# Kernel optimization log

Hardware: AMD Instinct MI355X
Metric: run time of the kernel (lower is better)

The kernel has to match this reference:

```python
import jax, jax.numpy as jnp
import numpy as np

MARGIN = 0.0
GAP = 0.4
N, D, C = 8192, 128, 10


def setup_inputs() -> dict:
    key = jax.random.key(0)
    k1, k2, k3 = jax.random.split(key, 3)
    inputs = jax.random.normal(k1, (N, D), dtype=jnp.float32)
    pred = jax.random.normal(k2, (N, C), dtype=jnp.float32)
    targets = jax.random.randint(k3, (N,), 0, C, dtype=jnp.int64)
    return {"inputs": inputs, "pred": pred, "targets": targets}


def reference(inputs, pred, targets):
    n = inputs.shape[0]
    # pairwise euclidean distances: ||xi||^2 + ||xj||^2 - 2 xi.xj, clamped + sqrt
    sq = jnp.sum(inputs * inputs, axis=1)                      # [n]
    dist = sq[:, None] + sq[None, :] - 2.0 * (inputs @ inputs.T)
    dist = jnp.sqrt(jnp.clip(dist, 1e-12))                     # [n, n]
    same = targets[:, None] == targets[None, :]                # [n, n] bool

    # confusion detection (original runs under no_grad)
    p = jax.nn.softmax(jax.lax.stop_gradient(pred), axis=1)
    val, top2 = jax.lax.top_k(p, 2)                            # [n,2]
    confuse = (val[:, 0] - val[:, 1] <= GAP) | (top2[:, 0] != targets)  # [n]

    # hard mining per row: hardest positive (max over same-class), hardest negative (min over diff-class)
    dist_ap = jnp.max(jnp.where(same, dist, -jnp.inf), axis=1)  # [n]
    dist_an = jnp.min(jnp.where(same, jnp.inf, dist), axis=1)   # [n]

    # MarginRankingLoss(margin=MARGIN) with y=1: mean(relu(-(an - ap) + margin)) over confused rows
    per_row = jnp.maximum(dist_ap - dist_an + MARGIN, 0.0)
    cnt = jnp.sum(confuse.astype(jnp.float32))
    loss = jnp.sum(jnp.where(confuse, per_row, 0.0)) / jnp.maximum(cnt, 1.0)
    return jnp.where(cnt > 0, loss, 0.0)
```

## Files before the change

kernel.cpp:

```cpp
#include <hip/hip_runtime.h>

#define NROWS 8192
#define DIMX  128
#define KB    192
#define KSEG  12
#define PTB   24576
#define NKS   3
#define NCLS  10
#define GAPV  0.4f
#define DEBIAS 504.03125f
#define SCL   (-0.0078125f)
#define RGR   256
#define NRG   (NROWS / RGR)
#define CHUNK 512
#define NCHUNK (NROWS / CHUNK)
#define SLAB  64
#define NSLAB (CHUNK / SLAB)

typedef __attribute__((ext_vector_type(4))) int i32x4;

#define GLOAD_LDS16(g, l)                                              \
  __builtin_amdgcn_global_load_lds(                                    \
      (const __attribute__((address_space(1))) void*)(g),              \
      (__attribute__((address_space(3))) void*)(l), 16, 0, 0)

__device__ __forceinline__ int q8(float v) {
  int q = (int)rintf(16.f * v);
  return q > 127 ? 127 : (q < -127 ? -127 : q);
}

__global__ __launch_bounds__(256) void prep_k(const float* __restrict__ x,
                                              const int* __restrict__ tgt,
                                              const float* __restrict__ pred,
                                              char* __restrict__ xa,
                                              char* __restrict__ xbm,
                                              float* __restrict__ sq,
                                              int* __restrict__ conf,
                                              unsigned* __restrict__ ctrs) {
  if (blockIdx.x == 0 && threadIdx.x < 3) ctrs[threadIdx.x] = 0u;

  const int wave = threadIdx.x >> 6;
  const int lane = threadIdx.x & 63;
  const int row  = blockIdx.x * 4 + wave;
  const float2 f2 = ((const float2*)(x + (size_t)row * DIMX))[lane];
  float s = f2.x * f2.x + f2.y * f2.y;
  #pragma unroll
  for (int m = 1; m < 64; m <<= 1) s += __shfl_xor(s, m, 64);

  char* basea = xa  + (size_t)(row >> 7) * PTB + (size_t)(row & 127) * 16;
  char* baseb = xbm + (size_t)(row >> 7) * PTB + (size_t)(row & 127) * 16;
  {
    const int q0 = q8(f2.x), q1 = q8(f2.y);
    const unsigned short u = (unsigned short)((q0 & 0xFF) | ((q1 & 0xFF) << 8));
    const size_t off = (size_t)(lane >> 3) * 2048 + (lane & 7) * 2;
    *(unsigned short*)(basea + off) = u;
    *(unsigned short*)(baseb + off) = u;
  }
  const int cls = tgt[row];
  if (lane < 32) {
    const int j = 2 * lane;
    const int c = j >> 2;
    const bool hit = (c < NCLS) && (c == cls);
    const unsigned short ua = hit ? (unsigned short)0x7F7F : 0;
    const unsigned short ub = hit ? (unsigned short)0x8181 : 0;
    const size_t off = (size_t)(8 + (j >> 4)) * 2048 + (j & 15);
    *(unsigned short*)(basea + off) = ua;
    *(unsigned short*)(baseb + off) = ub;
  }

  if (lane == 0) {
    sq[row] = s;
    const float* pp = pred + (size_t)row * NCLS;
    float v[NCLS];
    #pragma unroll
    for (int c = 0; c < NCLS; ++c) v[c] = pp[c];
    float m1 = v[0]; int i1 = 0;
    #pragma unroll
    for (int c = 1; c < NCLS; ++c)
      if (v[c] > m1) { m1 = v[c]; i1 = c; }
    float m2 = -INFINITY, sum = 0.f;
    #pragma unroll
    for (int c = 0; c < NCLS; ++c) {
      sum += __expf(v[c] - m1);
      if (c != i1) m2 = fmaxf(m2, v[c]);
    }
    const float d01 = (1.f - __expf(m2 - m1)) / sum;
    conf[row] = (d01 <= GAPV) || (i1 != cls);
  }
}

__global__ __launch_bounds__(256, 2) void gram_k(const char* __restrict__ xa,
                                                 const char* __restrict__ xbm,
                                                 const float* __restrict__ sq,
                                                 float* __restrict__ smax,
                                                 float* __restrict__ smin) {
  __shared__ char  ldsb[2][KSEG * 1024];
  __shared__ float sqb[2][SLAB];
  const int tid  = threadIdx.x;
  const int wave = tid >> 6;
  const int lane = tid & 63;
  const int quad = lane >> 4;
  const int m16  = lane & 15;
  const int bx = blockIdx.x, by = blockIdx.y;

  i32x4 A[4][NKS];
  #pragma unroll
  for (int rt = 0; rt < 4; ++rt) {
    const int rbase = wave * 64 + rt * 16;
    const char* pa = xa + (size_t)(bx * 2 + (rbase >> 7)) * PTB
                        + (size_t)((rbase & 127) + m16) * 16;
    #pragma unroll
    for (int ks = 0; ks < NKS; ++ks)
      A[rt][ks] = *(const i32x4*)(pa + (size_t)(ks * 4 + quad) * 2048);
  }
  #pragma unroll
  for (int rt = 0; rt < 4; ++rt)
    #pragma unroll
    for (int ks = 0; ks < NKS; ++ks)
      asm("" : "+v"(A[rt][ks]));

  float gmin[4][4], gmax[4][4];
  #pragma unroll
  for (int r = 0; r < 4; ++r)
    #pragma unroll
    for (int q = 0; q < 4; ++q) { gmin[r][q] = INFINITY; gmax[r][q] = -INFINITY; }

  {
    const char* srcb = xbm + (size_t)(by * 4) * PTB;
    #pragma unroll
    for (int u = 0; u < 3; ++u) {
      const int kseg = wave * 3 + u;
      GLOAD_LDS16(srcb + (size_t)kseg * 2048 + lane * 16, &ldsb[0][kseg * 1024 + lane * 16]);
    }
    if (wave == 3 && lane < 16)
      GLOAD_LDS16((const char*)(sq + by * CHUNK) + lane * 16, (char*)&sqb[0][0] + lane * 16);
  }

  for (int s = 0; s < NSLAB; ++s) {
    __syncthreads();
    if (s + 1 < NSLAB) {
      const char* srcb = xbm + (size_t)(by * 4 + ((s + 1) >> 1)) * PTB + ((s + 1) & 1) * 1024;
      char* dstb = &ldsb[(s + 1) & 1][0];
      #pragma unroll
      for (int u = 0; u < 3; ++u) {
        const int kseg = wave * 3 + u;
        GLOAD_LDS16(srcb + (size_t)kseg * 2048 + lane * 16, dstb + kseg * 1024 + lane * 16);
      }
      if (wave == 3 && lane < 16)
        GLOAD_LDS16((const char*)(sq + by * CHUNK + (s + 1) * SLAB) + lane * 16,
                    (char*)&sqb[(s + 1) & 1][0] + lane * 16);
    }
    const char* buf = &ldsb[s & 1][0];
    #pragma unroll
    for (int jt = 0; jt < 4; ++jt) {
      i32x4 B[NKS];
      #pragma unroll
      for (int ks = 0; ks < NKS; ++ks)
        B[ks] = *(const i32x4*)(buf + (ks * 4 + quad) * 1024 + (jt * 16 + m16) * 16);
      const float sqj = sqb[s & 1][jt * 16 + m16];

      i32x4 acc[4];
      #pragma unroll
      for (int r = 0; r < 4; ++r) acc[r] = (i32x4){0, 0, 0, 0};
      #pragma unroll
      for (int ks = 0; ks < NKS; ++ks)
        #pragma unroll
        for (int r = 0; r < 4; ++r)
          acc[r] = __builtin_amdgcn_mfma_i32_16x16x64_i8(A[r][ks], B[ks], acc[r], 0, 0, 0);

      #pragma unroll
      for (int r = 0; r < 4; ++r)
        #pragma unroll
        for (int q = 0; q < 4; ++q) {
          const float cand = fmaf((float)acc[r][q], SCL, sqj);
          gmin[r][q] = fminf(gmin[r][q], cand);
          gmax[r][q] = fmaxf(gmax[r][q], cand);
        }
    }
  }

  #pragma unroll
  for (int m = 1; m <= 8; m <<= 1)
    #pragma unroll
    for (int r = 0; r < 4; ++r)
      #pragma unroll
      for (int q = 0; q < 4; ++q) {
        gmin[r][q] = fminf(gmin[r][q], __shfl_xor(gmin[r][q], m, 64));
        gmax[r][q] = fmaxf(gmax[r][q], __shfl_xor(gmax[r][q], m, 64));
      }

  if (m16 == 0) {
    const size_t sidx = (size_t)(bx * NCHUNK + by) * RGR;
    #pragma unroll
    for (int r = 0; r < 4; ++r) {
      const int lrow = wave * 64 + r * 16 + quad * 4;
      *(float4*)&smax[sidx + lrow] = make_float4(gmax[r][0], gmax[r][1], gmax[r][2], gmax[r][3]);
      *(float4*)&smin[sidx + lrow] = make_float4(gmin[r][0], gmin[r][1], gmin[r][2], gmin[r][3]);
    }
  }
}

__global__ __launch_bounds__(256) void reduce_k(const float* __restrict__ smax,
                                                const float* __restrict__ smin,
                                                const float* __restrict__ sq,
                                                const int* __restrict__ conf,
                                                unsigned* __restrict__ ctrs,
                                                float* __restrict__ out) {
  __shared__ float red[2][4];
  const int tid = threadIdx.x, bx = blockIdx.x;
  const int wave = tid >> 6, lane = tid & 63;
  const int row = bx * RGR + tid;

  unsigned* g_done = ctrs;
  float*    Ssum   = (float*)(ctrs + 1);
  float*    Csum   = (float*)(ctrs + 2);

  float hi = -INFINITY, lo = INFINITY;
  #pragma unroll
  for (int c = 0; c < NCHUNK; ++c) {
    hi = fmaxf(hi, smax[(size_t)(bx * NCHUNK + c) * RGR + tid]);
    lo = fminf(lo, smin[(size_t)(bx * NCHUNK + c) * RGR + tid]);
  }
  float ps = 0.f, pc = 0.f;
  if (conf[row]) {
    const float ap = sqrtf(fmaxf(sq[row] + hi - DEBIAS, 1e-12f));
    const float an = sqrtf(fmaxf(sq[row] + lo, 1e-12f));
    ps = fmaxf(ap - an, 0.f);
    pc = 1.f;
  }
  #pragma unroll
  for (int m = 1; m < 64; m <<= 1) {
    ps += __shfl_xor(ps, m, 64);
    pc += __shfl_xor(pc, m, 64);
  }
  if (lane == 0) { red[0][wave] = ps; red[1][wave] = pc; }
  __syncthreads();
  if (tid == 0) {
    atomicAdd(Ssum, red[0][0] + red[0][1] + red[0][2] + red[0][3]);
    atomicAdd(Csum, red[1][0] + red[1][1] + red[1][2] + red[1][3]);
    __threadfence();
    if (atomicAdd(g_done, 1u) == NRG - 1u) {
      const float St = atomicAdd(Ssum, 0.f);
      const float Ct = atomicAdd(Csum, 0.f);
      out[0] = (Ct > 0.f) ? (St / fmaxf(Ct, 1.f)) : 0.f;
    }
  }
}

extern "C" void kernel_launch(void* const* d_in, const int* in_sizes, int n_in,
                              void* d_out, int out_size, void* d_ws, size_t ws_size,
                              hipStream_t stream) {
  const float* x    = (const float*)d_in[0];
  const float* pred = (const float*)d_in[1];
  const int*   tgt  = (const int*)d_in[2];
  float* out = (float*)d_out;

  char* w = (char*)d_ws;
  const size_t arr_bytes = (size_t)NROWS * KB;
  const size_t stg_bytes = (size_t)NRG * NCHUNK * RGR * 4;
  char*     xa   = w;
  char*     xbm  = w + arr_bytes;
  float*    sq   = (float*)(w + 2 * arr_bytes);
  int*      conf = (int*)(w + 2 * arr_bytes + (size_t)NROWS * 4);
  float*    smax = (float*)(w + 2 * arr_bytes + (size_t)NROWS * 8);
  float*    smin = (float*)(w + 2 * arr_bytes + (size_t)NROWS * 8 + stg_bytes);
  unsigned* ctrs = (unsigned*)(w + 2 * arr_bytes + (size_t)NROWS * 8 + 2 * stg_bytes);

  hipLaunchKernelGGL(prep_k, dim3(NROWS / 4), dim3(256), 0, stream,
                     x, tgt, pred, xa, xbm, sq, conf, ctrs);
  hipLaunchKernelGGL(gram_k, dim3(NRG, NCHUNK), dim3(256), 0, stream,
                     xa, xbm, sq, smax, smin);
  hipLaunchKernelGGL(reduce_k, dim3(NRG), dim3(256), 0, stream,
                     smax, smin, sq, conf, ctrs, out);
}
```

Measured before the change: 84.61 us.

## Exploit Gram matrix symmetry to compute only upper-triangular tiles

Switches the Gram kernel to square 256x256 tiles and launches only about half of the tile pairs, using a cyclic (bx+by) mapping so each unordered pair of row and column groups is visited once. Each off-diagonal tile also reduces per-column min/max across its rows, with the row squared norms held in registers, and writes these as the partials of the transposed tile. This roughly halves the int8 MFMA work and the B-operand traffic. In exchange it adds cross-lane shuffles, LDS column buffers, an extra barrier and epilogue per tile, and a reduce kernel that now reads twice as many partial chunks.

Result: slower. 106.0 us (+25.3%).

```diff
diff --git a/kernel.cpp b/kernel.cpp
--- a/kernel.cpp
+++ b/kernel.cpp
@@ -10,12 +10,10 @@
 #define GAPV  0.4f
 #define DEBIAS 504.03125f
 #define SCL   (-0.0078125f)
-#define RGR   256
-#define NRG   (NROWS / RGR)
-#define CHUNK 512
-#define NCHUNK (NROWS / CHUNK)
-#define SLAB  64
-#define NSLAB (CHUNK / SLAB)
+#define TG    256
+#define NG    (NROWS / TG)
+#define SLAB  128
+#define NSLAB (TG / SLAB)
 
 typedef __attribute__((ext_vector_type(4))) int i32x4;
 
@@ -94,20 +92,28 @@
                                                  const float* __restrict__ sq,
                                                  float* __restrict__ smax,
                                                  float* __restrict__ smin) {
-  __shared__ char  ldsb[2][KSEG * 1024];
+  const int bx = blockIdx.x, by = blockIdx.y;
+  if (by == 16 && bx >= 16) return;
+  const int rg = bx;
+  const int cg = (bx + by) & (NG - 1);
+  const bool do_col = (cg != rg);
+
+  __shared__ char  ldsb[2][KSEG * 2048];
   __shared__ float sqb[2][SLAB];
+  __shared__ float colmn[4][TG], colmx[4][TG];
   const int tid  = threadIdx.x;
   const int wave = tid >> 6;
   const int lane = tid & 63;
   const int quad = lane >> 4;
   const int m16  = lane & 15;
-  const int bx = blockIdx.x, by = blockIdx.y;
+  const int i0 = rg * TG;
+  const int j0 = cg * TG;
 
   i32x4 A[4][NKS];
   #pragma unroll
   for (int rt = 0; rt < 4; ++rt) {
     const int rbase = wave * 64 + rt * 16;
-    const char* pa = xa + (size_t)(bx * 2 + (rbase >> 7)) * PTB
+    const char* pa = xa + (size_t)(rg * 2 + (rbase >> 7)) * PTB
                         + (size_t)((rbase & 127) + m16) * 16;
     #pragma unroll
     for (int ks = 0; ks < NKS; ++ks)
@@ -119,6 +125,13 @@
     for (int ks = 0; ks < NKS; ++ks)
       asm("" : "+v"(A[rt][ks]));
 
+  float sqa[4][4];
+  #pragma unroll
+  for (int rt = 0; rt < 4; ++rt)
+    #pragma unroll
+    for (int q = 0; q < 4; ++q)
+      sqa[rt][q] = sq[i0 + wave * 64 + rt * 16 + quad * 4 + q];
+
   float gmin[4][4], gmax[4][4];
   #pragma unroll
   for (int r = 0; r < 4; ++r)
@@ -126,37 +139,39 @@
     for (int q = 0; q < 4; ++q) { gmin[r][q] = INFINITY; gmax[r][q] = -INFINITY; }
 
   {
-    const char* srcb = xbm + (size_t)(by * 4) * PTB;
+    const char* srcb = xbm + (size_t)(cg * 2) * PTB;
     #pragma unroll
     for (int u = 0; u < 3; ++u) {
       const int kseg = wave * 3 + u;
-      GLOAD_LDS16(srcb + (size_t)kseg * 2048 + lane * 16, &ldsb[0][kseg * 1024 + lane * 16]);
-    }
-    if (wave == 3 && lane < 16)
-      GLOAD_LDS16((const char*)(sq + by * CHUNK) + lane * 16, (char*)&sqb[0][0] + lane * 16);
+      GLOAD_LDS16(srcb + (size_t)kseg * 2048 + lane * 16, &ldsb[0][kseg * 2048 + lane * 16]);
+      GLOAD_LDS16(srcb + (size_t)kseg * 2048 + 1024 + lane * 16, &ldsb[0][kseg * 2048 + 1024 + lane * 16]);
+    }
+    if (wave == 3 && lane < 32)
+      GLOAD_LDS16((const char*)(sq + j0) + lane * 16, (char*)&sqb[0][0] + lane * 16);
   }
 
   for (int s = 0; s < NSLAB; ++s) {
     __syncthreads();
     if (s + 1 < NSLAB) {
-      const char* srcb = xbm + (size_t)(by * 4 + ((s + 1) >> 1)) * PTB + ((s + 1) & 1) * 1024;
+      const char* srcb = xbm + (size_t)(cg * 2 + s + 1) * PTB;
       char* dstb = &ldsb[(s + 1) & 1][0];
       #pragma unroll
       for (int u = 0; u < 3; ++u) {
         const int kseg = wave * 3 + u;
-        GLOAD_LDS16(srcb + (size_t)kseg * 2048 + lane * 16, dstb + kseg * 1024 + lane * 16);
+        GLOAD_LDS16(srcb + (size_t)kseg * 2048 + lane * 16, dstb + kseg * 2048 + lane * 16);
+        GLOAD_LDS16(srcb + (size_t)kseg * 2048 + 1024 + lane * 16, dstb + kseg * 2048 + 1024 + lane * 16);
       }
-      if (wave == 3 && lane < 16)
-        GLOAD_LDS16((const char*)(sq + by * CHUNK + (s + 1) * SLAB) + lane * 16,
+      if (wave == 3 && lane < 32)
+        GLOAD_LDS16((const char*)(sq + j0 + (s + 1) * SLAB) + lane * 16,
                     (char*)&sqb[(s + 1) & 1][0] + lane * 16);
     }
     const char* buf = &ldsb[s & 1][0];
     #pragma unroll
-    for (int jt = 0; jt < 4; ++jt) {
+    for (int jt = 0; jt < SLAB / 16; ++jt) {
       i32x4 B[NKS];
       #pragma unroll
       for (int ks = 0; ks < NKS; ++ks)
-        B[ks] = *(const i32x4*)(buf + (ks * 4 + quad) * 1024 + (jt * 16 + m16) * 16);
+        B[ks] = *(const i32x4*)(buf + (ks * 4 + quad) * 2048 + (jt * 16 + m16) * 16);
       const float sqj = sqb[s & 1][jt * 16 + m16];
 
       i32x4 acc[4];
@@ -176,6 +191,24 @@
           gmin[r][q] = fminf(gmin[r][q], cand);
           gmax[r][q] = fmaxf(gmax[r][q], cand);
         }
+      if (do_col) {
+        float cm = INFINITY, cx = -INFINITY;
+        #pragma unroll
+        for (int r = 0; r < 4; ++r)
+          #pragma unroll
+          for (int q = 0; q < 4; ++q) {
+            const float c2 = fmaf((float)acc[r][q], SCL, sqa[r][q]);
+            cm = fminf(cm, c2);
+            cx = fmaxf(cx, c2);
+          }
+        cm = fminf(cm, __shfl_xor(cm, 16, 64)); cm = fminf(cm, __shfl_xor(cm, 32, 64));
+        cx = fmaxf(cx, __shfl_xor(cx, 16, 64)); cx = fmaxf(cx, __shfl_xor(cx, 32, 64));
+        if (quad == 0) {
+          const int scol = s * SLAB + jt * 16 + m16;
+          colmn[wave][scol] = cm;
+          colmx[wave][scol] = cx;
+        }
+      }
     }
   }
 
@@ -188,15 +221,23 @@
         gmin[r][q] = fminf(gmin[r][q], __shfl_xor(gmin[r][q], m, 64));
         gmax[r][q] = fmaxf(gmax[r][q], __shfl_xor(gmax[r][q], m, 64));
       }
-
   if (m16 == 0) {
-    const size_t sidx = (size_t)(bx * NCHUNK + by) * RGR;
+    const size_t sidx = (size_t)(rg * NG + cg) * TG;
     #pragma unroll
     for (int r = 0; r < 4; ++r) {
       const int lrow = wave * 64 + r * 16 + quad * 4;
       *(float4*)&smax[sidx + lrow] = make_float4(gmax[r][0], gmax[r][1], gmax[r][2], gmax[r][3]);
       *(float4*)&smin[sidx + lrow] = make_float4(gmin[r][0], gmin[r][1], gmin[r][2], gmin[r][3]);
     }
+  }
+
+  if (do_col) {
+    __syncthreads();
+    const size_t tidx = (size_t)(cg * NG + rg) * TG + tid;
+    smin[tidx] = fminf(fminf(colmn[0][tid], colmn[1][tid]),
+                       fminf(colmn[2][tid], colmn[3][tid]));
+    smax[tidx] = fmaxf(fmaxf(colmx[0][tid], colmx[1][tid]),
+                       fmaxf(colmx[2][tid], colmx[3][tid]));
   }
 }
 
@@ -209,7 +250,7 @@
   __shared__ float red[2][4];
   const int tid = threadIdx.x, bx = blockIdx.x;
   const int wave = tid >> 6, lane = tid & 63;
-  const int row = bx * RGR + tid;
+  const int row = bx * TG + tid;
 
   unsigned* g_done = ctrs;
   float*    Ssum   = (float*)(ctrs + 1);
@@ -217,9 +258,9 @@
 
   float hi = -INFINITY, lo = INFINITY;
   #pragma unroll
-  for (int c = 0; c < NCHUNK; ++c) {
-    hi = fmaxf(hi, smax[(size_t)(bx * NCHUNK + c) * RGR + tid]);
-    lo = fminf(lo, smin[(size_t)(bx * NCHUNK + c) * RGR + tid]);
+  for (int c = 0; c < NG; ++c) {
+    hi = fmaxf(hi, smax[(size_t)(bx * NG + c) * TG + tid]);
+    lo = fminf(lo, smin[(size_t)(bx * NG + c) * TG + tid]);
   }
   float ps = 0.f, pc = 0.f;
   if (conf[row]) {
@@ -239,7 +280,7 @@
     atomicAdd(Ssum, red[0][0] + red[0][1] + red[0][2] + red[0][3]);
     atomicAdd(Csum, red[1][0] + red[1][1] + red[1][2] + red[1][3]);
     __threadfence();
-    if (atomicAdd(g_done, 1u) == NRG - 1u) {
+    if (atomicAdd(g_done, 1u) == NG - 1u) {
       const float St = atomicAdd(Ssum, 0.f);
       const float Ct = atomicAdd(Csum, 0.f);
       out[0] = (Ct > 0.f) ? (St / fmaxf(Ct, 1.f)) : 0.f;
@@ -257,7 +298,7 @@
 
   char* w = (char*)d_ws;
   const size_t arr_bytes = (size_t)NROWS * KB;
-  const size_t stg_bytes = (size_t)NRG * NCHUNK * RGR * 4;
+  const size_t stg_bytes = (size_t)NG * NG * TG * 4;
   char*     xa   = w;
   char*     xbm  = w + arr_bytes;
   float*    sq   = (float*)(w + 2 * arr_bytes);
@@ -268,8 +309,8 @@
 
   hipLaunchKernelGGL(prep_k, dim3(NROWS / 4), dim3(256), 0, stream,
                      x, tgt, pred, xa, xbm, sq, conf, ctrs);
-  hipLaunchKernelGGL(gram_k, dim3(NRG, NCHUNK), dim3(256), 0, stream,
+  hipLaunchKernelGGL(gram_k, dim3(NG, 17), dim3(256), 0, stream,
                      xa, xbm, sq, smax, smin);
-  hipLaunchKernelGGL(reduce_k, dim3(NRG), dim3(256), 0, stream,
+  hipLaunchKernelGGL(reduce_k, dim3(NG), dim3(256), 0, stream,
                      smax, smin, sq, conf, ctrs, out);
 }
```
